# Kernel optimization log

Hardware: AMD Instinct MI355X
Metric: run time of the kernel (lower is better)

The kernel has to match this reference:

```python
import jax, jax.numpy as jnp
import numpy as np

N, E = 50000, 800000
IN, H, D = 64, 4, 16          # in_feats, num_heads, head_size (IN == H*D -> identity skip)
NT, ET = 2, 2                 # num node / edge types


def setup_inputs() -> dict:
    key = jax.random.key(0)
    ks = jax.random.split(key, 13)
    s = 0.05
    return {
        "x": jax.random.normal(ks[0], (N, IN), jnp.float32),
        # TypedLinear weights: one [in,out] matrix per node type (DGL TypedLinear, no bias)
        "Wk": jax.random.normal(ks[1], (NT, IN, H * D), jnp.float32) * s,
        "Wq": jax.random.normal(ks[2], (NT, IN, H * D), jnp.float32) * s,
        "Wv": jax.random.normal(ks[3], (NT, IN, H * D), jnp.float32) * s,
        "Wa": jax.random.normal(ks[4], (NT, H * D, H * D), jnp.float32) * s,
        # per-head, per-edge-type relation matrices (relation_att / relation_msg)
        "Ratt": jax.random.normal(ks[5], (H, ET, D, D), jnp.float32) * s,
        "Rmsg": jax.random.normal(ks[6], (H, ET, D, D), jnp.float32) * s,
        "pri": jnp.ones((H, ET), jnp.float32),   # relation_pri
        "skip": jnp.ones((NT,), jnp.float32),    # skip gate per node type
        "ntype": jax.random.randint(ks[7], (N,), 0, NT),
        "etype": jax.random.randint(ks[8], (E,), 0, ET),
        "src": jax.random.randint(ks[9], (E,), 0, N),
        "dst": jax.random.randint(ks[10], (E,), 0, N),
    }


def _typed_linear(x, W, types):
    # x:[N,I], W:[T,I,O], types:[N] -> y[n] = x[n] @ W[types[n]]
    # T is tiny (2): compute all types densely, then select per node.
    y_all = jnp.einsum('ni,tio->tno', x, W)
    return y_all[types, jnp.arange(x.shape[0])]


def reference(x, Wk, Wq, Wv, Wa, Ratt, Rmsg, pri, skip, ntype, etype, src, dst):
    n = x.shape[0]
    k = _typed_linear(x, Wk, ntype).reshape(n, H, D)
    q = _typed_linear(x, Wq, ntype).reshape(n, H, D)
    v = _typed_linear(x, Wv, ntype).reshape(n, H, D)
    # relation transforms per edge type, computed once at node level (ET is tiny),
    # then gathered per edge: equivalent to per-edge TypedLinear in DGL's message fn.
    katt = jnp.einsum('nhd,htdf->thnf', k, Ratt)   # [ET,H,N,D]
    vmsg = jnp.einsum('nhd,htdf->thnf', v, Rmsg)   # [ET,H,N,D]
    kw = katt[etype, :, src]                       # [E,H,D]
    m = vmsg[etype, :, src]                        # [E,H,D]
    qd = q[dst]                                    # [E,H,D]
    # attention logits: (K W_att) . Q * relation_pri / sqrt(d)
    a = (kw * qd).sum(-1) * pri[:, etype].T / jnp.sqrt(jnp.float32(D))  # [E,H]
    # edge softmax over incoming edges of each destination node (stable)
    amax = jax.ops.segment_max(a, dst, num_segments=n)                  # [N,H]
    ae = jnp.exp(a - amax[dst])
    asum = jax.ops.segment_sum(ae, dst, num_segments=n)
    attn = ae / asum[dst]                                               # [E,H]
    # scatter-aggregate messages
    h = jax.ops.segment_sum(m * attn[:, :, None], dst, num_segments=n)  # [N,H,D]
    # target-specific output projection (dropout is identity in eval)
    h = _typed_linear(h.reshape(n, H * D), Wa, ntype)                   # [N,H*D]
    # sigmoid-gated skip (in_feats == H*D so identity residual)
    alpha = jax.nn.sigmoid(skip)[ntype][:, None]
    return h * alpha + x * (1.0 - alpha)
```

## Files before the change

kernel.cpp:

```cpp
#include <hip/hip_runtime.h>
#include <math.h>
#include <stdint.h>

#define N_NODES 50000
#define N_EDGES 800000
#define NT_TYPES 2
#define ET_TYPES 2
#define NB_SCAN ((N_NODES + 255) / 256)
#define M_COLS 320
#define M_PER_T (64 * M_COLS)
#define PROJ_GRID ((N_NODES + 63) / 64)
#define FILL_GRID ((N_EDGES + 255) / 256)
#define AGG_GRID ((N_NODES + 15) / 16)
#define MAXDEG 64
#define LOG2E 1.44269504088896f
#define HSTRIDE 36

typedef __attribute__((ext_vector_type(8))) short short8v;
typedef __attribute__((ext_vector_type(4))) float float4v;

__device__ __forceinline__ unsigned int f32_to_bf16(float f) {
  unsigned int u = __float_as_uint(f);
  return (u + 0x7FFFu + ((u >> 16) & 1u)) >> 16;
}

__device__ __forceinline__ float row16_sum(float p) {
  int r;
  r = __builtin_amdgcn_update_dpp(0, __float_as_int(p), 0x128, 0xf, 0xf, false);
  p += __int_as_float(r);
  r = __builtin_amdgcn_update_dpp(0, __float_as_int(p), 0x124, 0xf, 0xf, false);
  p += __int_as_float(r);
  r = __builtin_amdgcn_update_dpp(0, __float_as_int(p), 0x122, 0xf, 0xf, false);
  p += __int_as_float(r);
  r = __builtin_amdgcn_update_dpp(0, __float_as_int(p), 0x121, 0xf, 0xf, false);
  p += __int_as_float(r);
  return p;
}

__global__ void zero_kernel(int* __restrict__ deg) {
  const int i = blockIdx.x * 256 + threadIdx.x;
  if (i < N_NODES + 2) deg[i] = 0;
}

__global__ void prep_build_kernel(
    const float* __restrict__ Wk, const float* __restrict__ Wq,
    const float* __restrict__ Wv, const float* __restrict__ Wa,
    const float* __restrict__ Ratt, const float* __restrict__ Rmsg,
    const float* __restrict__ pri,
    const int* __restrict__ dst, const int* __restrict__ ntype,
    const float* __restrict__ x,
    unsigned short* __restrict__ M2b, unsigned short* __restrict__ Wa2b,
    int* __restrict__ deg, int* __restrict__ rank, int* __restrict__ tcnt,
    int* __restrict__ tlist, unsigned int* __restrict__ xb) {
  const int e = blockIdx.x * 256 + threadIdx.x;
  if (e < N_EDGES) rank[e] = atomicAdd(&deg[dst[e]], 1);
  if (e < N_NODES * 16) {
    float4 xa = reinterpret_cast<const float4*>(x)[e];
    xb[2 * e]     = f32_to_bf16(xa.x) | (f32_to_bf16(xa.y) << 16);
    xb[2 * e + 1] = f32_to_bf16(xa.z) | (f32_to_bf16(xa.w) << 16);
  }
  if (e < NT_TYPES * 4096) {
    int t = e >> 12;
    int rem = e & 4095;
    int col = rem >> 6, k = rem & 63;
    Wa2b[e] = (unsigned short)f32_to_bf16(Wa[(size_t)t * 4096 + k * 64 + col]);
  }
  if (e < NT_TYPES * M_PER_T) {
    int t = e / M_PER_T;
    int rem = e % M_PER_T;
    int col = rem / 64;
    int k = rem % 64;
    float val;
    if (col < 64) {
      val = Wq[(size_t)t * 4096 + k * 64 + col];
    } else {
      int cc = col - 64;
      int et = cc >> 7;
      int r = cc & 127;
      int c = r >> 1;
      int half = r & 1;
      int h = c >> 4, f = c & 15;
      const float* W = half ? Wv : Wk;
      const float* R = half ? Rmsg : Ratt;
      float s = 0.f;
#pragma unroll
      for (int d = 0; d < 16; ++d)
        s = fmaf(W[(size_t)t * 4096 + k * 64 + h * 16 + d],
                 R[(((size_t)h * ET_TYPES + et) * 16 + d) * 16 + f], s);
      if (half == 0) s *= pri[h * ET_TYPES + et] * 0.25f * LOG2E;
      val = s;
    }
    M2b[e] = (unsigned short)f32_to_bf16(val);
  }
  if (blockIdx.x < NB_SCAN) {
    __shared__ int lcnt[NT_TYPES];
    __shared__ int lbase[NT_TYPES];
    if (threadIdx.x < NT_TYPES) lcnt[threadIdx.x] = 0;
    __syncthreads();
    int t = 0, lpos = 0;
    const bool valid = (e < N_NODES);
    if (valid) {
      t = ntype[e];
      lpos = atomicAdd(&lcnt[t], 1);
    }
    __syncthreads();
    if (threadIdx.x < NT_TYPES)
      lbase[threadIdx.x] = atomicAdd(&tcnt[threadIdx.x], lcnt[threadIdx.x]);
    __syncthreads();
    if (valid)
      tlist[t * N_NODES + lbase[t] + lpos] = e;
  }
}

__global__ __launch_bounds__(256) void projfill_kernel(
    const unsigned short* __restrict__ xb,
    const unsigned short* __restrict__ M2b,
    const int* __restrict__ tcnt, const int* __restrict__ tlist,
    unsigned short* __restrict__ qb, unsigned int* __restrict__ kvb,
    const int* __restrict__ src, const int* __restrict__ dst,
    const int* __restrict__ etype, const int* __restrict__ rank,
    int* __restrict__ csr) {
  const int bid = blockIdx.x;
  if (bid >= 2 * PROJ_GRID) {
    const int e = (bid - 2 * PROJ_GRID) * 256 + threadIdx.x;
    if (e < N_EDGES) {
      int pos = (dst[e] << 6) + rank[e];
      __builtin_nontemporal_store((etype[e] * N_NODES + src[e]) << 6, &csr[pos]);
    }
    return;
  }
  const int ty = bid & 1;
  const int pb = bid >> 1;
  const int wave = threadIdx.x >> 6;
  const int lane = threadIdx.x & 63;
  const int cnt = __builtin_amdgcn_readfirstlane(tcnt[ty]);
  const int base = (pb * 4 + wave) * 16;
  if (base >= cnt) return;

  const int* lst = tlist + ty * N_NODES;
  const int l15 = lane & 15;
  const int lq = lane >> 4;

  const int nidA = lst[min(base + l15, cnt - 1)];
  const short8v A0 = *reinterpret_cast<const short8v*>(
      xb + (size_t)nidA * 64 + lq * 8);
  const short8v A1 = *reinterpret_cast<const short8v*>(
      xb + (size_t)nidA * 64 + 32 + lq * 8);

  const int n0 = lst[min(base + lq * 4 + 0, cnt - 1)];
  const int n1 = lst[min(base + lq * 4 + 1, cnt - 1)];
  const int n2 = lst[min(base + lq * 4 + 2, cnt - 1)];
  const int n3 = lst[min(base + lq * 4 + 3, cnt - 1)];

  const unsigned short* Bb = M2b + (size_t)ty * M_PER_T;

#pragma unroll
  for (int ct = 0; ct < 20; ++ct) {
    const int colb = ct * 16 + l15;
    const short8v B0 = *reinterpret_cast<const short8v*>(
        Bb + (size_t)colb * 64 + lq * 8);
    const short8v B1 = *reinterpret_cast<const short8v*>(
        Bb + (size_t)colb * 64 + 32 + lq * 8);
    float4v C = {0.f, 0.f, 0.f, 0.f};
    C = __builtin_amdgcn_mfma_f32_16x16x32_bf16(A0, B0, C, 0, 0, 0);
    C = __builtin_amdgcn_mfma_f32_16x16x32_bf16(A1, B1, C, 0, 0, 0);

    if (ct < 4) {
      qb[(size_t)n0 * 64 + colb] = (unsigned short)f32_to_bf16(C[0]);
      qb[(size_t)n1 * 64 + colb] = (unsigned short)f32_to_bf16(C[1]);
      qb[(size_t)n2 * 64 + colb] = (unsigned short)f32_to_bf16(C[2]);
      qb[(size_t)n3 * 64 + colb] = (unsigned short)f32_to_bf16(C[3]);
    } else {
      const float p0 = __shfl_xor(C[0], 1, 64);
      const float p1 = __shfl_xor(C[1], 1, 64);
      const float p2 = __shfl_xor(C[2], 1, 64);
      const float p3 = __shfl_xor(C[3], 1, 64);
      if ((lane & 1) == 0) {
        const int cc = colb - 64;
        const int et = cc >> 7;
        const int c = (cc & 127) >> 1;
        const size_t b0 = ((size_t)et * N_NODES) * 64 + c;
        kvb[b0 + (size_t)n0 * 64] = f32_to_bf16(C[0]) | (f32_to_bf16(p0) << 16);
        kvb[b0 + (size_t)n1 * 64] = f32_to_bf16(C[1]) | (f32_to_bf16(p1) << 16);
        kvb[b0 + (size_t)n2 * 64] = f32_to_bf16(C[2]) | (f32_to_bf16(p2) << 16);
        kvb[b0 + (size_t)n3 * 64] = f32_to_bf16(C[3]) | (f32_to_bf16(p3) << 16);
      }
    }
  }
}

__device__ __forceinline__ void edge_update(unsigned int wrd, float qd,
                                            float& srun, float& acc) {
  float kw = __uint_as_float(wrd << 16);
  float mv = __uint_as_float(wrd & 0xFFFF0000u);
  float w = __builtin_amdgcn_exp2f(row16_sum(kw * qd));
  srun += w;
  acc = fmaf(mv, w, acc);
}

__global__ __launch_bounds__(256) void agg_out_kernel(
    const unsigned short* __restrict__ qb, const unsigned int* __restrict__ kvb,
    const int* __restrict__ deg, const int* __restrict__ csr,
    const unsigned short* __restrict__ Wa2b, const float* __restrict__ x,
    const float* __restrict__ skip, const int* __restrict__ tcnt,
    const int* __restrict__ tlist, float* __restrict__ out) {
  __shared__ unsigned int hlds[16 * HSTRIDE];
  const int wave = threadIdx.x >> 6;
  const int lane = threadIdx.x & 63;
  const int ty = blockIdx.y;
  const int cnt = __builtin_amdgcn_readfirstlane(tcnt[ty]);
  const int base = blockIdx.x * 16;
  if (base >= cnt) return;
  const int* lst = tlist + ty * N_NODES;

  for (int r = 0; r < 4; ++r) {
    const int lrow = wave * 4 + r;
    int n = lst[min(base + lrow, cnt - 1)];
    n = __builtin_amdgcn_readfirstlane(n);
    const float qd = __uint_as_float((unsigned int)qb[(size_t)n * 64 + lane] << 16);
    const int ecnt = __builtin_amdgcn_readfirstlane(deg[n]);
    const int* crow = csr + (n << 6);

    float srun = 0.f, acc = 0.f;
    int j = 0;
    for (; j + 8 <= ecnt; j += 8) {
      int pk0 = __builtin_amdgcn_readfirstlane(crow[j + 0]);
      int pk1 = __builtin_amdgcn_readfirstlane(crow[j + 1]);
      int pk2 = __builtin_amdgcn_readfirstlane(crow[j + 2]);
      int pk3 = __builtin_amdgcn_readfirstlane(crow[j + 3]);
      int pk4 = __builtin_amdgcn_readfirstlane(crow[j + 4]);
      int pk5 = __builtin_amdgcn_readfirstlane(crow[j + 5]);
      int pk6 = __builtin_amdgcn_readfirstlane(crow[j + 6]);
      int pk7 = __builtin_amdgcn_readfirstlane(crow[j + 7]);
      unsigned int w0 = kvb[(unsigned)pk0 + lane];
      unsigned int w1 = kvb[(unsigned)pk1 + lane];
      unsigned int w2 = kvb[(unsigned)pk2 + lane];
      unsigned int w3 = kvb[(unsigned)pk3 + lane];
      unsigned int w4 = kvb[(unsigned)pk4 + lane];
      unsigned int w5 = kvb[(unsigned)pk5 + lane];
      unsigned int w6 = kvb[(unsigned)pk6 + lane];
      unsigned int w7 = kvb[(unsigned)pk7 + lane];
      edge_update(w0, qd, srun, acc);
      edge_update(w1, qd, srun, acc);
      edge_update(w2, qd, srun, acc);
      edge_update(w3, qd, srun, acc);
      edge_update(w4, qd, srun, acc);
      edge_update(w5, qd, srun, acc);
      edge_update(w6, qd, srun, acc);
      edge_update(w7, qd, srun, acc);
    }
    for (; j + 4 <= ecnt; j += 4) {
      int pk0 = __builtin_amdgcn_readfirstlane(crow[j + 0]);
      int pk1 = __builtin_amdgcn_readfirstlane(crow[j + 1]);
      int pk2 = __builtin_amdgcn_readfirstlane(crow[j + 2]);
      int pk3 = __builtin_amdgcn_readfirstlane(crow[j + 3]);
      unsigned int w0 = kvb[(unsigned)pk0 + lane];
      unsigned int w1 = kvb[(unsigned)pk1 + lane];
      unsigned int w2 = kvb[(unsigned)pk2 + lane];
      unsigned int w3 = kvb[(unsigned)pk3 + lane];
      edge_update(w0, qd, srun, acc);
      edge_update(w1, qd, srun, acc);
      edge_update(w2, qd, srun, acc);
      edge_update(w3, qd, srun, acc);
    }
    for (; j < ecnt; ++j) {
      int pk = __builtin_amdgcn_readfirstlane(crow[j]);
      unsigned int wd = kvb[(unsigned)pk + lane];
      edge_update(wd, qd, srun, acc);
    }
    float hv = (srun > 0.f) ? (acc / srun) : 0.f;
    float partner = __shfl_xor(hv, 1, 64);
    if ((lane & 1) == 0)
      hlds[lrow * HSTRIDE + (lane >> 1)] =
          f32_to_bf16(hv) | (f32_to_bf16(partner) << 16);
  }
  __syncthreads();

  const int l15 = lane & 15;
  const int lq = lane >> 4;
  const short8v A0 = *reinterpret_cast<const short8v*>(&hlds[l15 * HSTRIDE + lq * 4]);
  const short8v A1 = *reinterpret_cast<const short8v*>(&hlds[l15 * HSTRIDE + 16 + lq * 4]);

  const int n0 = lst[min(base + lq * 4 + 0, cnt - 1)];
  const int n1 = lst[min(base + lq * 4 + 1, cnt - 1)];
  const int n2 = lst[min(base + lq * 4 + 2, cnt - 1)];
  const int n3 = lst[min(base + lq * 4 + 3, cnt - 1)];

  const float alpha = 1.f / (1.f + __expf(-skip[ty]));
  const float beta = 1.f - alpha;
  const unsigned short* Bb = Wa2b + (size_t)ty * 4096;

  const int colb = wave * 16 + l15;
  const short8v B0 = *reinterpret_cast<const short8v*>(
      Bb + (size_t)colb * 64 + lq * 8);
  const short8v B1 = *reinterpret_cast<const short8v*>(
      Bb + (size_t)colb * 64 + 32 + lq * 8);
  float4v C = {0.f, 0.f, 0.f, 0.f};
  C = __builtin_amdgcn_mfma_f32_16x16x32_bf16(A0, B0, C, 0, 0, 0);
  C = __builtin_amdgcn_mfma_f32_16x16x32_bf16(A1, B1, C, 0, 0, 0);

  const size_t o0 = (size_t)n0 * 64 + colb;
  const size_t o1 = (size_t)n1 * 64 + colb;
  const size_t o2 = (size_t)n2 * 64 + colb;
  const size_t o3 = (size_t)n3 * 64 + colb;
  out[o0] = C[0] * alpha + x[o0] * beta;
  out[o1] = C[1] * alpha + x[o1] * beta;
  out[o2] = C[2] * alpha + x[o2] * beta;
  out[o3] = C[3] * alpha + x[o3] * beta;
}

extern "C" void kernel_launch(void* const* d_in, const int* in_sizes, int n_in,
                              void* d_out, int out_size, void* d_ws, size_t ws_size,
                              hipStream_t stream) {
  const float* x    = (const float*)d_in[0];
  const float* Wk   = (const float*)d_in[1];
  const float* Wq   = (const float*)d_in[2];
  const float* Wv   = (const float*)d_in[3];
  const float* Wa   = (const float*)d_in[4];
  const float* Ratt = (const float*)d_in[5];
  const float* Rmsg = (const float*)d_in[6];
  const float* pri  = (const float*)d_in[7];
  const float* skip = (const float*)d_in[8];
  const int* ntype  = (const int*)d_in[9];
  const int* etype  = (const int*)d_in[10];
  const int* src    = (const int*)d_in[11];
  const int* dst    = (const int*)d_in[12];
  float* out = (float*)d_out;

  unsigned short* qb = (unsigned short*)d_ws;
  unsigned int* kvb = (unsigned int*)(qb + (size_t)N_NODES * 64);
  unsigned short* xb = (unsigned short*)(kvb + (size_t)ET_TYPES * N_NODES * 64);
  int* deg   = (int*)(xb + (size_t)N_NODES * 64);
  int* tcnt  = deg + N_NODES;
  int* rank  = tcnt + 2;
  int* tlist = rank + N_EDGES;
  int* csr   = tlist + 2 * N_NODES;
  unsigned short* M2b = (unsigned short*)
      (((uintptr_t)(csr + (size_t)N_NODES * MAXDEG) + 255) & ~(uintptr_t)255);
  unsigned short* Wa2b = (unsigned short*)
      (((uintptr_t)(M2b + NT_TYPES * M_PER_T) + 255) & ~(uintptr_t)255);

  zero_kernel<<<NB_SCAN, 256, 0, stream>>>(deg);

  prep_build_kernel<<<FILL_GRID, 256, 0, stream>>>(
      Wk, Wq, Wv, Wa, Ratt, Rmsg, pri, dst, ntype, x,
      M2b, Wa2b, deg, rank, tcnt, tlist, (unsigned int*)xb);

  projfill_kernel<<<2 * PROJ_GRID + FILL_GRID, 256, 0, stream>>>(
      xb, M2b, tcnt, tlist, qb, kvb, src, dst, etype, rank, csr);

  dim3 agrid(AGG_GRID, NT_TYPES);
  agg_out_kernel<<<agrid, 256, 0, stream>>>(
      qb, (const unsigned int*)kvb, deg, csr, Wa2b, x, skip, tcnt, tlist, out);
}
```

Measured before the change: 123.3 us.

## Write CSR directly at atomic rank and interleave two destination nodes per wave

The CSR slot is now written immediately after the atomic degree increment in the prep kernel. This removes the rank array round-trip and the separate fill blocks in the projection kernel. The aggregation loop now processes two destination nodes per wave at once, interleaving their gathers to expose more memory-level parallelism, with tail loops handling the unequal degrees. The cost is more registers and code in the aggregation kernel, and scattered csr writes now run inside the atomic kernel.

```diff
diff --git a/kernel.cpp b/kernel.cpp
--- a/kernel.cpp
+++ b/kernel.cpp
@@ -10,7 +10,7 @@
 #define M_COLS 320
 #define M_PER_T (64 * M_COLS)
 #define PROJ_GRID ((N_NODES + 63) / 64)
-#define FILL_GRID ((N_EDGES + 255) / 256)
+#define EDGE_GRID ((N_EDGES + 255) / 256)
 #define AGG_GRID ((N_NODES + 15) / 16)
 #define MAXDEG 64
 #define LOG2E 1.44269504088896f
@@ -47,13 +47,20 @@
     const float* __restrict__ Wv, const float* __restrict__ Wa,
     const float* __restrict__ Ratt, const float* __restrict__ Rmsg,
     const float* __restrict__ pri,
-    const int* __restrict__ dst, const int* __restrict__ ntype,
+    const int* __restrict__ dst, const int* __restrict__ src,
+    const int* __restrict__ etype, const int* __restrict__ ntype,
     const float* __restrict__ x,
     unsigned short* __restrict__ M2b, unsigned short* __restrict__ Wa2b,
-    int* __restrict__ deg, int* __restrict__ rank, int* __restrict__ tcnt,
-    int* __restrict__ tlist, unsigned int* __restrict__ xb) {
+    int* __restrict__ deg, int* __restrict__ tcnt,
+    int* __restrict__ tlist, unsigned int* __restrict__ xb,
+    int* __restrict__ csr) {
   const int e = blockIdx.x * 256 + threadIdx.x;
-  if (e < N_EDGES) rank[e] = atomicAdd(&deg[dst[e]], 1);
+  if (e < N_EDGES) {
+    int d = dst[e];
+    int r = atomicAdd(&deg[d], 1);
+    __builtin_nontemporal_store((etype[e] * N_NODES + src[e]) << 6,
+                                &csr[(d << 6) + r]);
+  }
   if (e < N_NODES * 16) {
     float4 xa = reinterpret_cast<const float4*>(x)[e];
     xb[2 * e]     = f32_to_bf16(xa.x) | (f32_to_bf16(xa.y) << 16);
@@ -112,25 +119,13 @@
   }
 }
 
-__global__ __launch_bounds__(256) void projfill_kernel(
+__global__ __launch_bounds__(256) void proj_kernel(
     const unsigned short* __restrict__ xb,
     const unsigned short* __restrict__ M2b,
     const int* __restrict__ tcnt, const int* __restrict__ tlist,
-    unsigned short* __restrict__ qb, unsigned int* __restrict__ kvb,
-    const int* __restrict__ src, const int* __restrict__ dst,
-    const int* __restrict__ etype, const int* __restrict__ rank,
-    int* __restrict__ csr) {
-  const int bid = blockIdx.x;
-  if (bid >= 2 * PROJ_GRID) {
-    const int e = (bid - 2 * PROJ_GRID) * 256 + threadIdx.x;
-    if (e < N_EDGES) {
-      int pos = (dst[e] << 6) + rank[e];
-      __builtin_nontemporal_store((etype[e] * N_NODES + src[e]) << 6, &csr[pos]);
-    }
-    return;
-  }
-  const int ty = bid & 1;
-  const int pb = bid >> 1;
+    unsigned short* __restrict__ qb, unsigned int* __restrict__ kvb) {
+  const int ty = blockIdx.x & 1;
+  const int pb = blockIdx.x >> 1;
   const int wave = threadIdx.x >> 6;
   const int lane = threadIdx.x & 63;
   const int cnt = __builtin_amdgcn_readfirstlane(tcnt[ty]);
@@ -213,66 +208,95 @@
   if (base >= cnt) return;
   const int* lst = tlist + ty * N_NODES;
 
-  for (int r = 0; r < 4; ++r) {
-    const int lrow = wave * 4 + r;
-    int n = lst[min(base + lrow, cnt - 1)];
-    n = __builtin_amdgcn_readfirstlane(n);
-    const float qd = __uint_as_float((unsigned int)qb[(size_t)n * 64 + lane] << 16);
-    const int ecnt = __builtin_amdgcn_readfirstlane(deg[n]);
-    const int* crow = csr + (n << 6);
-
-    float srun = 0.f, acc = 0.f;
+  for (int half = 0; half < 2; ++half) {
+    const int lrowA = wave * 4 + half * 2;
+    int nA = __builtin_amdgcn_readfirstlane(lst[min(base + lrowA, cnt - 1)]);
+    int nB = __builtin_amdgcn_readfirstlane(lst[min(base + lrowA + 1, cnt - 1)]);
+    const float qdA = __uint_as_float((unsigned int)qb[(size_t)nA * 64 + lane] << 16);
+    const float qdB = __uint_as_float((unsigned int)qb[(size_t)nB * 64 + lane] << 16);
+    const int eA = __builtin_amdgcn_readfirstlane(deg[nA]);
+    const int eB = __builtin_amdgcn_readfirstlane(deg[nB]);
+    const int* cA = csr + (nA << 6);
+    const int* cB = csr + (nB << 6);
+
+    float sA = 0.f, aA = 0.f, sB = 0.f, aB = 0.f;
+    const int m = min(eA, eB);
     int j = 0;
-    for (; j + 8 <= ecnt; j += 8) {
-      int pk0 = __builtin_amdgcn_readfirstlane(crow[j + 0]);
-      int pk1 = __builtin_amdgcn_readfirstlane(crow[j + 1]);
-      int pk2 = __builtin_amdgcn_readfirstlane(crow[j + 2]);
-      int pk3 = __builtin_amdgcn_readfirstlane(crow[j + 3]);
-      int pk4 = __builtin_amdgcn_readfirstlane(crow[j + 4]);
-      int pk5 = __builtin_amdgcn_readfirstlane(crow[j + 5]);
-      int pk6 = __builtin_amdgcn_readfirstlane(crow[j + 6]);
-      int pk7 = __builtin_amdgcn_readfirstlane(crow[j + 7]);
-      unsigned int w0 = kvb[(unsigned)pk0 + lane];
-      unsigned int w1 = kvb[(unsigned)pk1 + lane];
-      unsigned int w2 = kvb[(unsigned)pk2 + lane];
-      unsigned int w3 = kvb[(unsigned)pk3 + lane];
-      unsigned int w4 = kvb[(unsigned)pk4 + lane];
-      unsigned int w5 = kvb[(unsigned)pk5 + lane];
-      unsigned int w6 = kvb[(unsigned)pk6 + lane];
-      unsigned int w7 = kvb[(unsigned)pk7 + lane];
-      edge_update(w0, qd, srun, acc);
-      edge_update(w1, qd, srun, acc);
-      edge_update(w2, qd, srun, acc);
-      edge_update(w3, qd, srun, acc);
-      edge_update(w4, qd, srun, acc);
-      edge_update(w5, qd, srun, acc);
-      edge_update(w6, qd, srun, acc);
-      edge_update(w7, qd, srun, acc);
-    }
-    for (; j + 4 <= ecnt; j += 4) {
-      int pk0 = __builtin_amdgcn_readfirstlane(crow[j + 0]);
-      int pk1 = __builtin_amdgcn_readfirstlane(crow[j + 1]);
-      int pk2 = __builtin_amdgcn_readfirstlane(crow[j + 2]);
-      int pk3 = __builtin_amdgcn_readfirstlane(crow[j + 3]);
-      unsigned int w0 = kvb[(unsigned)pk0 + lane];
-      unsigned int w1 = kvb[(unsigned)pk1 + lane];
-      unsigned int w2 = kvb[(unsigned)pk2 + lane];
-      unsigned int w3 = kvb[(unsigned)pk3 + lane];
-      edge_update(w0, qd, srun, acc);
-      edge_update(w1, qd, srun, acc);
-      edge_update(w2, qd, srun, acc);
-      edge_update(w3, qd, srun, acc);
-    }
-    for (; j < ecnt; ++j) {
-      int pk = __builtin_amdgcn_readfirstlane(crow[j]);
-      unsigned int wd = kvb[(unsigned)pk + lane];
-      edge_update(wd, qd, srun, acc);
-    }
-    float hv = (srun > 0.f) ? (acc / srun) : 0.f;
-    float partner = __shfl_xor(hv, 1, 64);
-    if ((lane & 1) == 0)
-      hlds[lrow * HSTRIDE + (lane >> 1)] =
-          f32_to_bf16(hv) | (f32_to_bf16(partner) << 16);
+    for (; j + 4 <= m; j += 4) {
+      int pA0 = __builtin_amdgcn_readfirstlane(cA[j + 0]);
+      int pA1 = __builtin_amdgcn_readfirstlane(cA[j + 1]);
+      int pA2 = __builtin_amdgcn_readfirstlane(cA[j + 2]);
+      int pA3 = __builtin_amdgcn_readfirstlane(cA[j + 3]);
+      int pB0 = __builtin_amdgcn_readfirstlane(cB[j + 0]);
+      int pB1 = __builtin_amdgcn_readfirstlane(cB[j + 1]);
+      int pB2 = __builtin_amdgcn_readfirstlane(cB[j + 2]);
+      int pB3 = __builtin_amdgcn_readfirstlane(cB[j + 3]);
+      unsigned int wA0 = kvb[(unsigned)pA0 + lane];
+      unsigned int wA1 = kvb[(unsigned)pA1 + lane];
+      unsigned int wA2 = kvb[(unsigned)pA2 + lane];
+      unsigned int wA3 = kvb[(unsigned)pA3 + lane];
+      unsigned int wB0 = kvb[(unsigned)pB0 + lane];
+      unsigned int wB1 = kvb[(unsigned)pB1 + lane];
+      unsigned int wB2 = kvb[(unsigned)pB2 + lane];
+      unsigned int wB3 = kvb[(unsigned)pB3 + lane];
+      edge_update(wA0, qdA, sA, aA);
+      edge_update(wB0, qdB, sB, aB);
+      edge_update(wA1, qdA, sA, aA);
+      edge_update(wB1, qdB, sB, aB);
+      edge_update(wA2, qdA, sA, aA);
+      edge_update(wB2, qdB, sB, aB);
+      edge_update(wA3, qdA, sA, aA);
+      edge_update(wB3, qdB, sB, aB);
+    }
+    int jA = j;
+    for (; jA + 4 <= eA; jA += 4) {
+      int p0 = __builtin_amdgcn_readfirstlane(cA[jA + 0]);
+      int p1 = __builtin_amdgcn_readfirstlane(cA[jA + 1]);
+      int p2 = __builtin_amdgcn_readfirstlane(cA[jA + 2]);
+      int p3 = __builtin_amdgcn_readfirstlane(cA[jA + 3]);
+      unsigned int w0 = kvb[(unsigned)p0 + lane];
+      unsigned int w1 = kvb[(unsigned)p1 + lane];
+      unsigned int w2 = kvb[(unsigned)p2 + lane];
+      unsigned int w3 = kvb[(unsigned)p3 + lane];
+      edge_update(w0, qdA, sA, aA);
+      edge_update(w1, qdA, sA, aA);
+      edge_update(w2, qdA, sA, aA);
+      edge_update(w3, qdA, sA, aA);
+    }
+    for (; jA < eA; ++jA) {
+      int p = __builtin_amdgcn_readfirstlane(cA[jA]);
+      edge_update(kvb[(unsigned)p + lane], qdA, sA, aA);
+    }
+    int jB = j;
+    for (; jB + 4 <= eB; jB += 4) {
+      int p0 = __builtin_amdgcn_readfirstlane(cB[jB + 0]);
+      int p1 = __builtin_amdgcn_readfirstlane(cB[jB + 1]);
+      int p2 = __builtin_amdgcn_readfirstlane(cB[jB + 2]);
+      int p3 = __builtin_amdgcn_readfirstlane(cB[jB + 3]);
+      unsigned int w0 = kvb[(unsigned)p0 + lane];
+      unsigned int w1 = kvb[(unsigned)p1 + lane];
+      unsigned int w2 = kvb[(unsigned)p2 + lane];
+      unsigned int w3 = kvb[(unsigned)p3 + lane];
+      edge_update(w0, qdB, sB, aB);
+      edge_update(w1, qdB, sB, aB);
+      edge_update(w2, qdB, sB, aB);
+      edge_update(w3, qdB, sB, aB);
+    }
+    for (; jB < eB; ++jB) {
+      int p = __builtin_amdgcn_readfirstlane(cB[jB]);
+      edge_update(kvb[(unsigned)p + lane], qdB, sB, aB);
+    }
+
+    float hvA = (sA > 0.f) ? (aA / sA) : 0.f;
+    float hvB = (sB > 0.f) ? (aB / sB) : 0.f;
+    float prA = __shfl_xor(hvA, 1, 64);
+    float prB = __shfl_xor(hvB, 1, 64);
+    if ((lane & 1) == 0) {
+      hlds[lrowA * HSTRIDE + (lane >> 1)] =
+          f32_to_bf16(hvA) | (f32_to_bf16(prA) << 16);
+      hlds[(lrowA + 1) * HSTRIDE + (lane >> 1)] =
+          f32_to_bf16(hvB) | (f32_to_bf16(prB) << 16);
+    }
   }
   __syncthreads();
 
@@ -332,8 +356,7 @@
   unsigned short* xb = (unsigned short*)(kvb + (size_t)ET_TYPES * N_NODES * 64);
   int* deg   = (int*)(xb + (size_t)N_NODES * 64);
   int* tcnt  = deg + N_NODES;
-  int* rank  = tcnt + 2;
-  int* tlist = rank + N_EDGES;
+  int* tlist = tcnt + 2;
   int* csr   = tlist + 2 * N_NODES;
   unsigned short* M2b = (unsigned short*)
       (((uintptr_t)(csr + (size_t)N_NODES * MAXDEG) + 255) & ~(uintptr_t)255);
@@ -342,12 +365,12 @@
 
   zero_kernel<<<NB_SCAN, 256, 0, stream>>>(deg);
 
-  prep_build_kernel<<<FILL_GRID, 256, 0, stream>>>(
-      Wk, Wq, Wv, Wa, Ratt, Rmsg, pri, dst, ntype, x,
-      M2b, Wa2b, deg, rank, tcnt, tlist, (unsigned int*)xb);
-
-  projfill_kernel<<<2 * PROJ_GRID + FILL_GRID, 256, 0, stream>>>(
-      xb, M2b, tcnt, tlist, qb, kvb, src, dst, etype, rank, csr);
+  prep_build_kernel<<<EDGE_GRID, 256, 0, stream>>>(
+      Wk, Wq, Wv, Wa, Ratt, Rmsg, pri, dst, src, etype, ntype, x,
+      M2b, Wa2b, deg, tcnt, tlist, (unsigned int*)xb, csr);
+
+  proj_kernel<<<2 * PROJ_GRID, 256, 0, stream>>>(
+      xb, M2b, tcnt, tlist, qb, kvb);
 
   dim3 agrid(AGG_GRID, NT_TYPES);
   agg_out_kernel<<<agrid, 256, 0, stream>>>(
```

Result: no change. 123.8 us (+0.3%).
